# Optimization experiments

Measured on AMD Instinct MI355X. Metric: run time of the kernel, lower is better.

The kernel has to match this reference:

```python
import jax, jax.numpy as jnp
import numpy as np

N_PTS = 262144      # 512x512 coordinate grid
N_HEADS = 16
HID = 256
N_HID_LAYERS = 3
IN_F = 2
OUT_F = 3
PE_L = 10                  # NeRF positional-encoding frequencies
PE_DIM = 2 * IN_F * PE_L   # sin+cos per freq per coord = 40
CAP = N_PTS // N_HEADS     # balanced partition: points per head


def positional_encoding(x):
    # x: [..., IN_F] -> [..., PE_DIM]
    freqs = (2.0 ** jnp.arange(PE_L, dtype=x.dtype)) * jnp.pi          # [L]
    ang = x[..., None, :] * freqs[:, None]                              # [..., L, IN_F]
    pe = jnp.concatenate([jnp.sin(ang), jnp.cos(ang)], axis=-1)        # [..., L, 2*IN_F]
    return pe.reshape(*x.shape[:-1], PE_DIM)


def setup_inputs() -> dict:
    key = jax.random.key(0)
    ks = jax.random.split(key, 5)
    # Balanced random segment map (equivalent to the module's segment_weight),
    # converted to the static routing table the torch loop recomputes each step:
    # head_idx[h] = where(segment_weight == h)
    rng = np.random.default_rng(0)
    seg = rng.permutation(np.arange(N_PTS) % N_HEADS)
    head_idx = np.stack([np.where(seg == h)[0] for h in range(N_HEADS)]).astype(np.int32)  # [H, CAP]

    coords = jax.random.uniform(ks[0], (1, N_PTS, IN_F), minval=-1.0, maxval=1.0)

    def he(k, shape, fan_in):
        return jax.random.normal(k, shape, dtype=jnp.float32) * np.float32(np.sqrt(2.0 / fan_in))

    W_in = he(ks[1], (N_HEADS, PE_DIM, HID), PE_DIM)
    b_in = jnp.zeros((N_HEADS, HID), jnp.float32)
    W_hid = he(ks[2], (N_HEADS, N_HID_LAYERS, HID, HID), HID)
    b_hid = jnp.zeros((N_HEADS, N_HID_LAYERS, HID), jnp.float32)
    W_out = he(ks[3], (N_HEADS, HID, OUT_F), HID)
    b_out = jnp.zeros((N_HEADS, OUT_F), jnp.float32)

    return dict(coords=coords, head_idx=jnp.asarray(head_idx),
                W_in=W_in, b_in=b_in, W_hid=W_hid, b_hid=b_hid,
                W_out=W_out, b_out=b_out)


def reference(coords, head_idx, W_in, b_in, W_hid, b_hid, W_out, b_out):
    # --- dispatch: gather each head's points (torch: coords[:, index, :]) ---
    coords_h = coords[0][head_idx]                                      # [H, CAP, IN_F]
    # --- per-head MLP (relu_MLP with positional embedding) ---
    h = jax.nn.relu(jnp.einsum('hcd,hdf->hcf', positional_encoding(coords_h), W_in)
                    + b_in[:, None, :])                                 # [H, CAP, HID]
    for l in range(N_HID_LAYERS):
        h = jax.nn.relu(jnp.einsum('hcf,hfg->hcg', h, W_hid[:, l])
                        + b_hid[:, l, None, :])
    out_h = jnp.einsum('hcf,hfo->hco', h, W_out) + b_out[:, None, :]    # [H, CAP, OUT_F]
    # --- combine: scatter per-head outputs back (torch: output_final[0, index, :] = out) ---
    out_final = jnp.zeros((1, N_PTS, OUT_F), coords.dtype)
    out_final = out_final.at[0, head_idx.reshape(-1)].set(out_h.reshape(-1, OUT_F))
    return (out_final, coords)
```

## Files before the change

### kernel.cpp

```cpp
#include <hip/hip_runtime.h>

typedef unsigned short u16;
typedef unsigned int   u32;
typedef __bf16  bf16x8 __attribute__((ext_vector_type(8)));
typedef float   f32x16 __attribute__((ext_vector_type(16)));

#define CAP      16384
#define L0_ELS   (256*56)
#define HID_ELS  (256*256)
#define OUT_ELS  (32*256)
#define HEAD_WS  (L0_ELS + 3*HID_ELS + OUT_ELS)
#define HID_OFF  L0_ELS
#define OUT_OFF  (L0_ELS + 3*HID_ELS)

union F8 { u32 u[4]; bf16x8 v; };

__device__ __forceinline__ u16 f2b(float f) {
  u32 u = __float_as_uint(f); u += 0x7fffu + ((u >> 16) & 1u); return (u16)(u >> 16);
}
__device__ __forceinline__ u32 packbf2(float a, float b) {
  u32 ua = __float_as_uint(a); ua += 0x7fffu + ((ua >> 16) & 1u);
  u32 ub = __float_as_uint(b); ub += 0x7fffu + ((ub >> 16) & 1u);
  return (ua >> 16) | (ub & 0xffff0000u);
}

__device__ __forceinline__ f32x16 mfma16(bf16x8 a, bf16x8 b, f32x16 c) {
  return __builtin_amdgcn_mfma_f32_32x32x16_bf16(a, b, c, 0, 0, 0);
}

__device__ __forceinline__ void stage_now(const u16* g, short* l, int bytes, int tid) {
  for (int base = tid * 16; base < bytes; base += 8192)
    *(uint4*)((char*)l + base) = *(const uint4*)((const char*)g + base);
}
__device__ __forceinline__ void stage_ld(const u16* g, int bytes, int tid, uint4 st[4]) {
#pragma unroll
  for (int r = 0; r < 4; ++r) {
    const int base = tid * 16 + r * 8192;
    if (base < bytes) st[r] = *(const uint4*)((const char*)g + base);
  }
}
__device__ __forceinline__ void stage_st(short* l, int bytes, int tid, const uint4 st[4]) {
#pragma unroll
  for (int r = 0; r < 4; ++r) {
    const int base = tid * 16 + r * 8192;
    if (base < bytes) *(uint4*)((char*)l + base) = st[r];
  }
}

__device__ __forceinline__ bf16x8 fragL0(const short* sl, int i, int t, int n, int hh) {
  return *(const bf16x8*)((const char*)sl + (32*i + n)*112 + (2*t + hh)*16);
}
__device__ __forceinline__ bf16x8 fragH(const short* sl, int i, int t, int n, int hh) {
  return *(const bf16x8*)((const char*)sl + ((32*i + n) << 9) + (((2*t + hh) ^ (n & 7)) << 4));
}

__device__ __forceinline__ void load_bias_raw(const float* b, int r, int hh, float4 o[4]) {
#pragma unroll
  for (int g = 0; g < 4; ++g) o[g] = *(const float4*)(b + 32*r + 8*g + 4*hh);
}
__device__ __forceinline__ f32x16 bias_to_acc(const float4 raw[4]) {
  f32x16 a;
#pragma unroll
  for (int g = 0; g < 4; ++g) {
    a[4*g+0] = raw[g].x; a[4*g+1] = raw[g].y;
    a[4*g+2] = raw[g].z; a[4*g+3] = raw[g].w;
  }
  return a;
}

__device__ __forceinline__ void epilogue(f32x16 c, int hh, F8& t0, F8& t1) {
  u32 P[8];
#pragma unroll
  for (int i = 0; i < 8; ++i)
    P[i] = packbf2(fmaxf(c[2*i], 0.f), fmaxf(c[2*i+1], 0.f));
  u32 s0 = hh ? P[0] : P[2], s1 = hh ? P[1] : P[3];
  u32 s2 = hh ? P[4] : P[6], s3 = hh ? P[5] : P[7];
  u32 x0 = __shfl_xor(s0, 32, 64), x1 = __shfl_xor(s1, 32, 64);
  u32 x2 = __shfl_xor(s2, 32, 64), x3 = __shfl_xor(s3, 32, 64);
  t0.u[0] = hh ? x0 : P[0]; t0.u[1] = hh ? x1 : P[1];
  t0.u[2] = hh ? P[2] : x0; t0.u[3] = hh ? P[3] : x1;
  t1.u[0] = hh ? x2 : P[4]; t1.u[1] = hh ? x3 : P[5];
  t1.u[2] = hh ? P[6] : x2; t1.u[3] = hh ? P[7] : x3;
}

__global__ void prep(const float* __restrict__ W_in, const float* __restrict__ b_in,
                     const float* __restrict__ W_hid, const float* __restrict__ W_out,
                     u16* __restrict__ ws) {
  const int ct = blockIdx.x * 256 + threadIdx.x;
  const int head = ct / 27392;
  const int r = ct - head * 27392;
  u16 v[8]; int dst;
  if (r < 1792) {
    const int nn = r / 7, k0 = (r % 7) * 8;
#pragma unroll
    for (int j = 0; j < 8; ++j) {
      const int k = k0 + j;
      v[j] = (k < 40) ? f2b(W_in[head*10240 + k*256 + nn])
           : (k == 40) ? f2b(b_in[head*256 + nn]) : (u16)0;
    }
    dst = head*HEAD_WS + nn*56 + k0;
  } else if (r < 26368) {
    const int q = r - 1792, l = q >> 13, q2 = q & 8191;
    const int nn = q2 >> 5, cc = q2 & 31, kb = 8 * (cc ^ (nn & 7));
#pragma unroll
    for (int j = 0; j < 8; ++j)
      v[j] = f2b(W_hid[head*196608 + l*65536 + (kb + j)*256 + nn]);
    dst = head*HEAD_WS + HID_OFF + l*65536 + nn*256 + cc*8;
  } else {
    const int q = r - 26368;
    const int nn = q >> 5, cc = q & 31, kb = 8 * (cc ^ (nn & 7));
#pragma unroll
    for (int j = 0; j < 8; ++j)
      v[j] = (nn < 3) ? f2b(W_out[head*768 + (kb + j)*3 + nn]) : (u16)0;
    dst = head*HEAD_WS + OUT_OFF + nn*256 + cc*8;
  }
  uint4 o;
  o.x = (u32)v[0] | ((u32)v[1] << 16); o.y = (u32)v[2] | ((u32)v[3] << 16);
  o.z = (u32)v[4] | ((u32)v[5] << 16); o.w = (u32)v[6] | ((u32)v[7] << 16);
  *(uint4*)(ws + dst) = o;
}

__global__ void copy_coords(const uint4* __restrict__ s, uint4* __restrict__ d) {
  const int i = blockIdx.x * 256 + threadIdx.x;
  d[i] = s[i];
}

__launch_bounds__(512, 2)
__global__ void mlp_main(const float* __restrict__ coords, const int* __restrict__ head_idx,
                         const float* __restrict__ b_hid, const float* __restrict__ b_out,
                         const u16* __restrict__ ws, float* __restrict__ out) {
  __shared__ short ring[2 * 16384];
  const int tid = threadIdx.x;
  const int lane = tid & 63, wv = tid >> 6;
  const int n = lane & 31, hh = lane >> 5;
  const int head = blockIdx.x & 15, chunk = blockIdx.x >> 4;
  const u16* wsh = ws + head * HEAD_WS;

  stage_now(wsh + 0*3584, ring,          7168, tid);
  stage_now(wsh + 1*3584, ring + 16384,  7168, tid);

  const int pt = chunk*256 + wv*32 + n;
  const int g  = head_idx[head*CAP + pt];
  const float2 cxy = *(const float2*)(coords + 2*g);
  const float xs = cxy.x, ys = cxy.y;
  const float bo0 = b_out[head*3+0], bo1 = b_out[head*3+1], bo2 = b_out[head*3+2];

  F8 pe[3];
#pragma unroll
  for (int t = 0; t < 3; ++t) {
    float e[8];
#pragma unroll
    for (int half = 0; half < 2; ++half) {
      const int l = 4*t + 2*hh + half;
      if (l < 10) {
        const float fr = 3.14159265358979323846f * (float)(1 << l);
        float s1, c1, s2, c2;
        sincosf(xs * fr, &s1, &c1);
        sincosf(ys * fr, &s2, &c2);
        e[4*half+0] = s1; e[4*half+1] = s2; e[4*half+2] = c1; e[4*half+3] = c2;
      } else {
        e[4*half+0] = (l == 10) ? 1.0f : 0.0f;
        e[4*half+1] = 0.f; e[4*half+2] = 0.f; e[4*half+3] = 0.f;
      }
    }
    pe[t].u[0] = packbf2(e[0], e[1]); pe[t].u[1] = packbf2(e[2], e[3]);
    pe[t].u[2] = packbf2(e[4], e[5]); pe[t].u[3] = packbf2(e[6], e[7]);
  }

  F8 act0[16], act1[16];
  __syncthreads();

#pragma unroll
  for (int rp = 0; rp < 4; ++rp) {
    short* sl = ring + (rp & 1) * 16384;
    f32x16 acc0 = (f32x16)0.f, acc1 = (f32x16)0.f;
#pragma unroll
    for (int t = 0; t < 3; ++t) {
      acc0 = mfma16(fragL0(sl, 0, t, n, hh), pe[t].v, acc0);
      acc1 = mfma16(fragL0(sl, 1, t, n, hh), pe[t].v, acc1);
    }
    __syncthreads();
    const u16* src = (rp < 2) ? (wsh + (rp + 2)*3584) : (wsh + HID_OFF + (rp - 2)*16384);
    const int bytes = (rp < 2) ? 7168 : 32768;
    uint4 st[4];
    stage_ld(src, bytes, tid, st);
    epilogue(acc0, hh, act0[4*rp+0], act0[4*rp+1]);
    epilogue(acc1, hh, act0[4*rp+2], act0[4*rp+3]);
    stage_st(sl, bytes, tid, st);
  }

  auto hid_layer = [&](const float* bias, F8 (&ain)[16], F8 (&aout)[16],
                       const u16* j0, const u16* j1, const u16* j2, const u16* j3,
                       int b2, int b3) {
    float4 bc0[4], bc1[4], bn0[4], bn1[4];
    load_bias_raw(bias, 0, hh, bc0); load_bias_raw(bias, 1, hh, bc1);
    const u16* jsrc[4] = { j0, j1, j2, j3 };
    const int  jb[4]   = { 32768, 32768, b2, b3 };
#pragma unroll
    for (int rp = 0; rp < 4; ++rp) {
      short* sl = ring + (rp & 1) * 16384;
      if (rp < 3) { load_bias_raw(bias, 2*rp+2, hh, bn0); load_bias_raw(bias, 2*rp+3, hh, bn1); }
      f32x16 acc0 = bias_to_acc(bc0);
      f32x16 acc1 = bias_to_acc(bc1);
#pragma unroll
      for (int t = 0; t < 16; ++t) {
        bf16x8 a0 = fragH(sl, 0, t, n, hh);
        bf16x8 a1 = fragH(sl, 1, t, n, hh);
        acc0 = mfma16(a0, ain[t].v, acc0);
        acc1 = mfma16(a1, ain[t].v, acc1);
      }
      __syncthreads();
      uint4 st[4];
      if (jb[rp] > 0) stage_ld(jsrc[rp], jb[rp], tid, st);
      epilogue(acc0, hh, aout[4*rp+0], aout[4*rp+1]);
      epilogue(acc1, hh, aout[4*rp+2], aout[4*rp+3]);
      if (jb[rp] > 0) stage_st(sl, jb[rp], tid, st);
      if (rp < 3) {
#pragma unroll
        for (int q = 0; q < 4; ++q) { bc0[q] = bn0[q]; bc1[q] = bn1[q]; }
      }
    }
  };

  const u16* hb = wsh + HID_OFF;
  hid_layer(b_hid + (head*3+0)*256, act0, act1,
            hb + 2*16384, hb + 3*16384, hb + HID_ELS, hb + HID_ELS + 16384, 32768, 32768);
  hid_layer(b_hid + (head*3+1)*256, act1, act0,
            hb + HID_ELS + 2*16384, hb + HID_ELS + 3*16384,
            hb + 2*HID_ELS, hb + 2*HID_ELS + 16384, 32768, 32768);
  hid_layer(b_hid + (head*3+2)*256, act0, act1,
            hb + 2*HID_ELS + 2*16384, hb + 2*HID_ELS + 3*16384,
            wsh + OUT_OFF, (const u16*)0, 16384, 0);

  f32x16 acc = (f32x16)0.f;
#pragma unroll
  for (int t = 0; t < 16; ++t)
    acc = mfma16(fragH(ring, 0, t, n, hh), act1[t].v, acc);
  if (hh == 0) {
    const long base = (long)g * 3;
    out[base + 0] = acc[0] + bo0;
    out[base + 1] = acc[1] + bo1;
    out[base + 2] = acc[2] + bo2;
  }
}

extern "C" void kernel_launch(void* const* d_in, const int* in_sizes, int n_in,
                              void* d_out, int out_size, void* d_ws, size_t ws_size,
                              hipStream_t stream) {
  const float* coords   = (const float*)d_in[0];
  const int*   head_idx = (const int*)d_in[1];
  const float* W_in     = (const float*)d_in[2];
  const float* b_in     = (const float*)d_in[3];
  const float* W_hid    = (const float*)d_in[4];
  const float* b_hid    = (const float*)d_in[5];
  const float* W_out    = (const float*)d_in[6];
  const float* b_out    = (const float*)d_in[7];
  float* out = (float*)d_out;
  u16*   ws  = (u16*)d_ws;
  if (ws_size < (size_t)HEAD_WS * 16 * sizeof(u16)) return;

  prep<<<dim3(1712), dim3(256), 0, stream>>>(W_in, b_in, W_hid, W_out, ws);
  copy_coords<<<dim3(512), dim3(256), 0, stream>>>((const uint4*)coords, (uint4*)(out + 786432));
  mlp_main<<<dim3(1024), dim3(512), 0, stream>>>(coords, head_idx, b_hid, b_out, ws, out);
}
```

Measured before the change: 224.4 us.

## Stage weights with direct global-to-LDS loads and halve block size

Replaces the register-staged global→LDS weight copies with the global_load_lds builtin, so weight tiles stream straight into shared memory without a register round-trip. Blocks shrink from 512 to 256 threads and the grid doubles, so each block handles 128 points. The intent is to cut VGPR pressure and copy instructions. The risk is that no explicit vmcnt wait is visible before the __syncthreads that precedes consuming the ring buffer, which could be a correctness hazard. Halving the block also doubles how often each head's weights are reloaded into LDS.

Result: no change. 220.1 us (-1.9%).

```diff
diff --git a/kernel.cpp b/kernel.cpp
--- a/kernel.cpp
+++ b/kernel.cpp
@@ -28,23 +28,12 @@
   return __builtin_amdgcn_mfma_f32_32x32x16_bf16(a, b, c, 0, 0, 0);
 }
 
-__device__ __forceinline__ void stage_now(const u16* g, short* l, int bytes, int tid) {
-  for (int base = tid * 16; base < bytes; base += 8192)
-    *(uint4*)((char*)l + base) = *(const uint4*)((const char*)g + base);
-}
-__device__ __forceinline__ void stage_ld(const u16* g, int bytes, int tid, uint4 st[4]) {
-#pragma unroll
-  for (int r = 0; r < 4; ++r) {
-    const int base = tid * 16 + r * 8192;
-    if (base < bytes) st[r] = *(const uint4*)((const char*)g + base);
-  }
-}
-__device__ __forceinline__ void stage_st(short* l, int bytes, int tid, const uint4 st[4]) {
-#pragma unroll
-  for (int r = 0; r < 4; ++r) {
-    const int base = tid * 16 + r * 8192;
-    if (base < bytes) *(uint4*)((char*)l + base) = st[r];
-  }
+__device__ __forceinline__ void stage_async(const u16* __restrict__ g, short* l,
+                                            int bytes, int tid) {
+  for (int base = tid * 16; base < bytes; base += 4096)
+    __builtin_amdgcn_global_load_lds(
+        (const __attribute__((address_space(1))) u32*)((const char*)g + base),
+        (__attribute__((address_space(3))) u32*)((char*)l + base), 16, 0, 0);
 }
 
 __device__ __forceinline__ bf16x8 fragL0(const short* sl, int i, int t, int n, int hh) {
@@ -125,7 +114,7 @@
   d[i] = s[i];
 }
 
-__launch_bounds__(512, 2)
+__launch_bounds__(256, 2)
 __global__ void mlp_main(const float* __restrict__ coords, const int* __restrict__ head_idx,
                          const float* __restrict__ b_hid, const float* __restrict__ b_out,
                          const u16* __restrict__ ws, float* __restrict__ out) {
@@ -136,10 +125,10 @@
   const int head = blockIdx.x & 15, chunk = blockIdx.x >> 4;
   const u16* wsh = ws + head * HEAD_WS;
 
-  stage_now(wsh + 0*3584, ring,          7168, tid);
-  stage_now(wsh + 1*3584, ring + 16384,  7168, tid);
-
-  const int pt = chunk*256 + wv*32 + n;
+  stage_async(wsh + 0*3584, ring,          7168, tid);
+  stage_async(wsh + 1*3584, ring + 16384,  7168, tid);
+
+  const int pt = chunk*128 + wv*32 + n;
   const int g  = head_idx[head*CAP + pt];
   const float2 cxy = *(const float2*)(coords + 2*g);
   const float xs = cxy.x, ys = cxy.y;
@@ -182,11 +171,9 @@
     __syncthreads();
     const u16* src = (rp < 2) ? (wsh + (rp + 2)*3584) : (wsh + HID_OFF + (rp - 2)*16384);
     const int bytes = (rp < 2) ? 7168 : 32768;
-    uint4 st[4];
-    stage_ld(src, bytes, tid, st);
+    stage_async(src, sl, bytes, tid);
     epilogue(acc0, hh, act0[4*rp+0], act0[4*rp+1]);
     epilogue(acc1, hh, act0[4*rp+2], act0[4*rp+3]);
-    stage_st(sl, bytes, tid, st);
   }
 
   auto hid_layer = [&](const float* bias, F8 (&ain)[16], F8 (&aout)[16],
@@ -210,11 +197,9 @@
         acc1 = mfma16(a1, ain[t].v, acc1);
       }
       __syncthreads();
-      uint4 st[4];
-      if (jb[rp] > 0) stage_ld(jsrc[rp], jb[rp], tid, st);
+      if (jb[rp] > 0) stage_async(jsrc[rp], sl, jb[rp], tid);
       epilogue(acc0, hh, aout[4*rp+0], aout[4*rp+1]);
       epilogue(acc1, hh, aout[4*rp+2], aout[4*rp+3]);
-      if (jb[rp] > 0) stage_st(sl, jb[rp], tid, st);
       if (rp < 3) {
 #pragma unroll
         for (int q = 0; q < 4; ++q) { bc0[q] = bn0[q]; bc1[q] = bn1[q]; }
@@ -261,5 +246,5 @@
 
   prep<<<dim3(1712), dim3(256), 0, stream>>>(W_in, b_in, W_hid, W_out, ws);
   copy_coords<<<dim3(512), dim3(256), 0, stream>>>((const uint4*)coords, (uint4*)(out + 786432));
-  mlp_main<<<dim3(1024), dim3(512), 0, stream>>>(coords, head_idx, b_hid, b_out, ws, out);
-}
+  mlp_main<<<dim3(2048), dim3(256), 0, stream>>>(coords, head_idx, b_hid, b_out, ws, out);
+}
```
